# Kernel tuning notes

Measured on AMD Instinct MI355X. Metric: run time of the kernel, lower is better.

## Reference

```python
import jax, jax.numpy as jnp
import numpy as np

D_CONV = 4
DT_RANK = 64
D_STATE = 16

def silu(v):
    return v * jax.nn.sigmoid(v)

def setup_inputs() -> dict:
    key = jax.random.key(0)
    ks = jax.random.split(key, 10)
    B, L, d_model, d_inner = 2, 2048, 1024, 2048
    def nrm(k, shape, scale):
        return jax.random.normal(k, shape, dtype=jnp.float32) * scale
    A = jnp.tile(jnp.arange(1, D_STATE + 1, dtype=jnp.float32), (d_inner, 1))
    return {
        'x': nrm(ks[0], (B, L, d_model), 1.0),
        'W_in': nrm(ks[1], (d_model, 2 * d_inner), d_model ** -0.5),
        'conv_w': nrm(ks[2], (d_inner, D_CONV), D_CONV ** -0.5),
        'conv_b': nrm(ks[3], (d_inner,), 0.02),
        'W_x': nrm(ks[4], (d_inner, DT_RANK + 2 * D_STATE), d_inner ** -0.5),
        'W_dt': nrm(ks[5], (DT_RANK, d_inner), DT_RANK ** -0.5),
        'b_dt': nrm(ks[6], (d_inner,), 0.02),
        'A_log': jnp.log(A),
        'D': jnp.ones((d_inner,), dtype=jnp.float32),
        'W_out': nrm(ks[7], (d_inner, d_model), d_inner ** -0.5),
    }

def reference(x, W_in, conv_w, conv_b, W_x, W_dt, b_dt, A_log, D, W_out):
    B, L, _ = x.shape
    d_inner = W_dt.shape[1]
    # input projection and gate split
    xz = x @ W_in                                   # [B, L, 2*d_inner]
    xb, z = jnp.split(xz, 2, axis=-1)
    # causal depthwise conv1d (pad left d_conv-1, then first L outputs)
    xp = jnp.pad(xb, ((0, 0), (D_CONV - 1, 0), (0, 0)))
    xc = sum(xp[:, k:k + L, :] * conv_w[:, k] for k in range(D_CONV)) + conv_b
    xb = silu(xc)                                   # [B, L, d_inner]
    # data-dependent SSM parameters
    x_dbl = xb @ W_x                                # [B, L, dt_rank + 2*d_state]
    dt_low, Bm, Cm = jnp.split(x_dbl, [DT_RANK, DT_RANK + D_STATE], axis=-1)
    dt = jax.nn.softplus(dt_low @ W_dt + b_dt)      # [B, L, d_inner]
    A = -jnp.exp(A_log)                             # [d_inner, d_state]

    def step(h, inp):
        dt_t, B_t, C_t, x_t = inp                   # [B,d_inner],[B,n],[B,n],[B,d_inner]
        dA = jnp.exp(A * dt_t[..., None])           # [B, d_inner, d_state]
        h = h * dA + (x_t * dt_t)[..., None] * B_t[:, None, :]
        y = jnp.einsum('bdn,bn->bd', h, C_t)
        return h, y

    xs = (dt.swapaxes(0, 1), Bm.swapaxes(0, 1), Cm.swapaxes(0, 1), xb.swapaxes(0, 1))
    h0 = jnp.zeros((B, d_inner, D_STATE), dtype=x.dtype)
    _, ys = jax.lax.scan(step, h0, xs)              # ys: [L, B, d_inner]
    y = ys.swapaxes(0, 1) + xb * D
    out = y * silu(z)
    return out @ W_out
```

## Files before the change

kernel.cpp:

```cpp
#include <hip/hip_runtime.h>
#include <hip/hip_bf16.h>


#define BATCH   2
#define SEQLEN  2048
#define DMODEL  1024
#define DINNER  2048
#define DCONV   4
#define DTRANK  64
#define DSTATE  16
#define BL      (BATCH * SEQLEN)
#define NXZ     (2 * DINNER)
#define XDBL_N  (DTRANK + 2 * DSTATE)
#define LCH     32
#define NCHUNK  (SEQLEN / LCH)
#define KSPLIT  8
#define KC      (DINNER / KSPLIT)
#define KS_OUT  4
#define KCO     (DINNER / KS_OUT)
#define KS_XD   8
#define KCX     (DINNER / KS_XD)
#define XDP     128

typedef __bf16 bf16x8 __attribute__((ext_vector_type(8)));
typedef __bf16 bf16x4 __attribute__((ext_vector_type(4)));
typedef float  floatx4 __attribute__((ext_vector_type(4)));

__device__ __forceinline__ float silu_f(float v) {
    return v / (1.f + __expf(-v));
}

__device__ __forceinline__ float softplus_f(float v) {
    return (v > 20.f) ? v : __logf(1.f + __expf(v));
}

__device__ __forceinline__ float fast_exp2(float v) {
    return __builtin_amdgcn_exp2f(v);
}

__device__ __forceinline__ void gload_lds16(const __bf16* g, __bf16* l) {
    __builtin_amdgcn_global_load_lds(
        (const __attribute__((address_space(1))) void*)g,
        (__attribute__((address_space(3))) void*)l, 16, 0, 0);
}

#define VMW(n) asm volatile("s_waitcnt vmcnt(" #n ")" ::: "memory")
#define BARX() __builtin_amdgcn_s_barrier()

template <int BUF, int QA>
__device__ __forceinline__ void rdA(const char* rA, bf16x8 (&aF)[4][2]) {
#pragma unroll
    for (int j = 0; j < 4; ++j) {
        aF[j][0] = *(const bf16x8*)(rA + BUF * 65536 + ((QA * 4 + j) * 2 + 0) * 1024);
        aF[j][1] = *(const bf16x8*)(rA + BUF * 65536 + ((QA * 4 + j) * 2 + 1) * 1024);
    }
}

template <int BUF, int QB>
__device__ __forceinline__ void rdB(const char* rB, bf16x8 (&bF)[2][2]) {
#pragma unroll
    for (int f = 0; f < 2; ++f) {
        bF[f][0] = *(const bf16x8*)(rB + BUF * 65536 + QB * 8192 + f * 2048 + 0);
        bF[f][1] = *(const bf16x8*)(rB + BUF * 65536 + QB * 8192 + f * 2048 + 1024);
    }
}

template <int QA, int QB>
__device__ __forceinline__ void mf16(const bf16x8 (&aF)[4][2], const bf16x8 (&bF)[2][2],
                                     floatx4 (&acc)[8][4]) {
    __builtin_amdgcn_s_setprio(1);
#pragma unroll
    for (int ks = 0; ks < 2; ++ks)
#pragma unroll
        for (int j = 0; j < 4; ++j)
#pragma unroll
            for (int f = 0; f < 2; ++f)
                acc[QA * 4 + j][QB * 2 + f] = __builtin_amdgcn_mfma_f32_16x16x32_bf16(
                    aF[j][ks], bF[f][ks], acc[QA * 4 + j][QB * 2 + f], 0, 0, 0);
    __builtin_amdgcn_s_setprio(0);
}

template <int BUF, int QA>
__device__ __forceinline__ void stA2(const __bf16* gAs, char* sm, int lda, int w, int t) {
    gload_lds16(gAs + (size_t)(QA * 64) * lda + t * 64,
                (__bf16*)(sm + BUF * 65536 + QA * 8192 + w * 1024));
    gload_lds16(gAs + (size_t)(128 + QA * 64) * lda + t * 64,
                (__bf16*)(sm + BUF * 65536 + 16384 + QA * 8192 + w * 1024));
}

template <int BUF, int QB>
__device__ __forceinline__ void stB2(const __bf16* gBs, char* sm, int lda, int w, int t) {
    gload_lds16(gBs + (size_t)(QB * 32) * lda + t * 64,
                (__bf16*)(sm + BUF * 65536 + 32768 + QB * 8192 + w * 1024));
    gload_lds16(gBs + (size_t)(128 + QB * 32) * lda + t * 64,
                (__bf16*)(sm + BUF * 65536 + 32768 + 16384 + QB * 8192 + w * 1024));
}

template <int EPI>
__global__ __launch_bounds__(512, 2) void gemm_bt_256(
    const __bf16* __restrict__ A,
    const __bf16* __restrict__ BT,
    void* __restrict__ Cv,
    int M, int N, int K, int lda,
    const float* __restrict__ bias)
{
    __shared__ __align__(16) char smem[131072];

    const int tid  = threadIdx.x;
    const int w    = tid >> 6;
    const int lane = tid & 63;

    const int cpx = gridDim.x >> 3;
    const int swz = (blockIdx.x & 7) * cpx + (blockIdx.x >> 3);
    const int ntn = N >> 8;
    const int row0 = (swz / ntn) << 8;
    const int col0 = (swz % ntn) << 8;
    const int kbase = blockIdx.y * K;

    const int P     = tid;
    const int rr    = (P >> 2) & 15;
    const int qq    = (P & 3) ^ (2 * ((P >> 5) & 1));
    const int colE  = (((P >> 6) & 1) * 4 + qq) * 8;
    const int rgP   = P >> 7;
    const int rowAu = rgP * 16 + rr;
    const int rowBu = (rgP >> 1) * 64 + (rgP & 1) * 16 + rr;

    const __bf16* gAs = A  + (size_t)(row0 + rowAu) * lda + kbase + colE;
    const __bf16* gBs = BT + (size_t)(col0 + rowBu) * lda + kbase + colE;
    char* sm = smem;

    const int lsw = ((lane & 15) * 4 + ((lane >> 4) ^ (2 * ((lane >> 3) & 1)))) * 16;
    const char* rA = smem + (w >> 2) * 16384 + lsw;
    const char* rB = smem + 32768 + ((w & 3) >> 1) * 16384 + ((w & 3) & 1) * 4096 + lsw;

    floatx4 acc[8][4];
#pragma unroll
    for (int i = 0; i < 8; ++i)
#pragma unroll
        for (int j = 0; j < 4; ++j)
            acc[i][j] = (floatx4){0.f, 0.f, 0.f, 0.f};
    bf16x8 aF[4][2], bF[2][2];

    const int NT = K >> 6;
    const int NI = NT >> 1;

    stA2<0, 0>(gAs, sm, lda, w, 0);
    stB2<0, 0>(gBs, sm, lda, w, 0);
    stB2<0, 1>(gBs, sm, lda, w, 0);
    stA2<0, 1>(gAs, sm, lda, w, 0);
    stA2<1, 0>(gAs, sm, lda, w, 1);
    stB2<1, 1>(gBs, sm, lda, w, 1);
    VMW(6);
    BARX();

    for (int i = 0; i < NI - 1; ++i) {
        const int t1 = 2 * i + 1, t2 = 2 * i + 2, t3 = 2 * i + 3;
        rdA<0, 0>(rA, aF); rdB<0, 0>(rB, bF);
        stB2<1, 0>(gBs, sm, lda, w, t1);
        BARX(); mf16<0, 0>(aF, bF, acc); BARX();
        rdB<0, 1>(rB, bF);
        stA2<1, 1>(gAs, sm, lda, w, t1);
        BARX(); mf16<0, 1>(aF, bF, acc); VMW(8); BARX();
        rdA<0, 1>(rA, aF);
        stA2<0, 0>(gAs, sm, lda, w, t2);
        BARX(); mf16<1, 1>(aF, bF, acc); BARX();
        rdB<0, 0>(rB, bF);
        stB2<0, 1>(gBs, sm, lda, w, t2);
        BARX(); mf16<1, 0>(aF, bF, acc); VMW(6); BARX();
        rdA<1, 0>(rA, aF); rdB<1, 0>(rB, bF);
        stB2<0, 0>(gBs, sm, lda, w, t2);
        BARX(); mf16<0, 0>(aF, bF, acc); BARX();
        rdB<1, 1>(rB, bF);
        stA2<0, 1>(gAs, sm, lda, w, t2);
        BARX(); mf16<0, 1>(aF, bF, acc); VMW(8); BARX();
        rdA<1, 1>(rA, aF);
        stA2<1, 0>(gAs, sm, lda, w, t3);
        BARX(); mf16<1, 1>(aF, bF, acc); BARX();
        rdB<1, 0>(rB, bF);
        stB2<1, 1>(gBs, sm, lda, w, t3);
        BARX(); mf16<1, 0>(aF, bF, acc); VMW(6); BARX();
    }
    {
        const int t1 = NT - 1;
        rdA<0, 0>(rA, aF); rdB<0, 0>(rB, bF);
        stB2<1, 0>(gBs, sm, lda, w, t1);
        BARX(); mf16<0, 0>(aF, bF, acc); BARX();
        rdB<0, 1>(rB, bF);
        stA2<1, 1>(gAs, sm, lda, w, t1);
        BARX(); mf16<0, 1>(aF, bF, acc); VMW(8); BARX();
        rdA<0, 1>(rA, aF);
        BARX(); mf16<1, 1>(aF, bF, acc); BARX();
        rdB<0, 0>(rB, bF);
        BARX(); mf16<1, 0>(aF, bF, acc); VMW(2); BARX();
        rdA<1, 0>(rA, aF); rdB<1, 0>(rB, bF);
        BARX(); mf16<0, 0>(aF, bF, acc); BARX();
        rdB<1, 1>(rB, bF);
        BARX(); mf16<0, 1>(aF, bF, acc); VMW(0); BARX();
        rdA<1, 1>(rA, aF);
        BARX(); mf16<1, 1>(aF, bF, acc); BARX();
        rdB<1, 0>(rB, bF);
        BARX(); mf16<1, 0>(aF, bF, acc);
    }

    const int lrow = lane & 15, quad = lane >> 4;

    if (EPI == 2 || EPI == 3) {
        __syncthreads();
#pragma unroll
        for (int fi = 0; fi < 8; ++fi) {
#pragma unroll
            for (int cf = 0; cf < 4; ++cf) {
                const int lc = (w & 3) * 64 + cf * 16 + lrow;
                const float bv = (EPI == 3) ? bias[col0 + lc] : 0.f;
#pragma unroll
                for (int r = 0; r < 4; ++r) {
                    const int lr = (w >> 2) * 128 + fi * 16 + quad * 4 + r;
                    float v = acc[fi][cf][r];
                    if (EPI == 3) v = softplus_f(v + bv);
                    const int ck = (lc >> 3) ^ ((lr >> 2) & 7);
                    *(__bf16*)(smem + lr * 512 + ck * 16 + (lc & 7) * 2) = (__bf16)v;
                }
            }
        }
        __syncthreads();
#pragma unroll
        for (int it = 0; it < 16; ++it) {
            const int row = it * 16 + w * 2 + (lane >> 5);
            const int cr  = lane & 31;
            const int ck  = cr ^ ((row >> 2) & 7);
            bf16x8 v = *(const bf16x8*)(smem + row * 512 + ck * 16);
            *(bf16x8*)((__bf16*)Cv + (size_t)(row0 + row) * N + col0 + cr * 8) = v;
        }
    } else {
        const size_t cofs = (size_t)blockIdx.y * (size_t)M * (size_t)N;
        const int rbase = row0 + (w >> 2) * 128;
        const int cbase = col0 + (w & 3) * 64;
#pragma unroll
        for (int fi = 0; fi < 8; ++fi) {
#pragma unroll
            for (int cf = 0; cf < 4; ++cf) {
                const int col = cbase + cf * 16 + lrow;
                const float bv = (EPI == 1) ? bias[col] : 0.f;
#pragma unroll
                for (int r = 0; r < 4; ++r) {
                    const int row = rbase + fi * 16 + quad * 4 + r;
                    float v = acc[fi][cf][r];
                    if (EPI == 1) v = softplus_f(v + bv);
                    ((float*)Cv)[cofs + (size_t)row * N + col] = v;
                }
            }
        }
    }
    (void)M;
}

__global__ __launch_bounds__(256) void out_reduce(
    const float* __restrict__ parts, float* __restrict__ out)
{
    const size_t i = ((size_t)blockIdx.x * 256 + threadIdx.x) * 4;
    floatx4 s = *(const floatx4*)(parts + i);
#pragma unroll
    for (int kz = 1; kz < KS_OUT; ++kz)
        s += *(const floatx4*)(parts + (size_t)kz * BL * DMODEL + i);
    *(floatx4*)(out + i) = s;
}

template <int EPI>
__global__ __launch_bounds__(256) void gemm_r64(
    const __bf16* __restrict__ A,
    const __bf16* __restrict__ BT,
    void* __restrict__ Cv,
    int M, int N, int K,
    const float* __restrict__ bias)
{
    __shared__ __bf16 Asm[64 * 32];
    __shared__ __bf16 Bsm[128 * 32];

    const int tid  = threadIdx.x;
    const int w    = tid >> 6;
    const int lane = tid & 63;
    const int lrow = lane & 15;
    const int quad = lane >> 4;
    const int row0 = blockIdx.y * 64;
    const int col0 = blockIdx.x * 128;
    const int wc   = w * 32;

    const int ldr = tid >> 2;
    const int ldk = (tid & 3) * 8;
    const __bf16* gA = A  + (size_t)(row0 + ldr) * K + ldk;
    const __bf16* gB = BT + (size_t)(col0 + ldr) * K + ldk;
    const size_t half = (size_t)64 * K;
    __bf16* lA0 = Asm + w * 512;
    __bf16* lB0 = Bsm + w * 512;
    __bf16* lB1 = Bsm + 2048 + w * 512;

    floatx4 acc[4][2];
#pragma unroll
    for (int i = 0; i < 4; ++i)
#pragma unroll
        for (int j = 0; j < 2; ++j)
            acc[i][j] = (floatx4){0.f, 0.f, 0.f, 0.f};

    for (int k0 = 0; k0 < K; k0 += 32) {
        gload_lds16(gA, lA0);
        gload_lds16(gB, lB0);
        gload_lds16(gB + half, lB1);
        gA += 32; gB += 32;
        __syncthreads();

        bf16x8 af[4], bf[2];
#pragma unroll
        for (int t = 0; t < 4; ++t)
            af[t] = *(const bf16x8*)(Asm + (t * 16 + lrow) * 32 + quad * 8);
#pragma unroll
        for (int u = 0; u < 2; ++u)
            bf[u] = *(const bf16x8*)(Bsm + (wc + u * 16 + lrow) * 32 + quad * 8);

#pragma unroll
        for (int ti = 0; ti < 4; ++ti)
#pragma unroll
            for (int tj = 0; tj < 2; ++tj)
                acc[ti][tj] = __builtin_amdgcn_mfma_f32_16x16x32_bf16(
                    af[ti], bf[tj], acc[ti][tj], 0, 0, 0);
        __syncthreads();
    }

#pragma unroll
    for (int ti = 0; ti < 4; ++ti) {
#pragma unroll
        for (int tj = 0; tj < 2; ++tj) {
            int col = col0 + wc + tj * 16 + lrow;
            float bv = (EPI == 1 || EPI == 3) ? bias[col] : 0.f;
#pragma unroll
            for (int r = 0; r < 4; ++r) {
                int row = row0 + ti * 16 + quad * 4 + r;
                float v = acc[ti][tj][r];
                if (EPI == 1 || EPI == 3) v = softplus_f(v + bv);
                if (EPI == 2 || EPI == 3)
                    ((__bf16*)Cv)[(size_t)row * N + col] = (__bf16)v;
                else
                    ((float*)Cv)[(size_t)row * N + col] = v;
            }
        }
    }
}

__global__ __launch_bounds__(256) void xdbl_gemm(
    const __bf16* __restrict__ A,
    const __bf16* __restrict__ BT,
    float* __restrict__ parts)
{
    __shared__ __bf16 Asm[64 * 32];
    __shared__ __bf16 Bsm[128 * 32];

    const int tid  = threadIdx.x;
    const int w    = tid >> 6;
    const int lane = tid & 63;
    const int lrow = lane & 15;
    const int quad = lane >> 4;
    const int row0 = blockIdx.x * 64;
    const int kbeg = blockIdx.y * KCX;
    const int wc   = w * 32;

    const int ldr = tid >> 2;
    const int ldk = (tid & 3) * 8;
    const __bf16* gA = A  + (size_t)(row0 + ldr) * DINNER + kbeg + ldk;
    const __bf16* gB = BT + (size_t)ldr * DINNER + kbeg + ldk;
    const size_t half = (size_t)64 * DINNER;
    __bf16* lA0 = Asm + w * 512;
    __bf16* lB0 = Bsm + w * 512;
    __bf16* lB1 = Bsm + 2048 + w * 512;

    floatx4 acc[4][2];
#pragma unroll
    for (int i = 0; i < 4; ++i)
#pragma unroll
        for (int j = 0; j < 2; ++j)
            acc[i][j] = (floatx4){0.f, 0.f, 0.f, 0.f};

    for (int k0 = 0; k0 < KCX; k0 += 32) {
        gload_lds16(gA, lA0);
        gload_lds16(gB, lB0);
        gload_lds16(gB + half, lB1);
        gA += 32; gB += 32;
        __syncthreads();

        bf16x8 af[4], bf[2];
#pragma unroll
        for (int t = 0; t < 4; ++t)
            af[t] = *(const bf16x8*)(Asm + (t * 16 + lrow) * 32 + quad * 8);
#pragma unroll
        for (int u = 0; u < 2; ++u)
            bf[u] = *(const bf16x8*)(Bsm + (wc + u * 16 + lrow) * 32 + quad * 8);

#pragma unroll
        for (int ti = 0; ti < 4; ++ti)
#pragma unroll
            for (int tj = 0; tj < 2; ++tj)
                acc[ti][tj] = __builtin_amdgcn_mfma_f32_16x16x32_bf16(
                    af[ti], bf[tj], acc[ti][tj], 0, 0, 0);
        __syncthreads();
    }

    const size_t base = (size_t)blockIdx.y * BL * XDP;
#pragma unroll
    for (int ti = 0; ti < 4; ++ti) {
#pragma unroll
        for (int tj = 0; tj < 2; ++tj) {
            int col = wc + tj * 16 + lrow;
#pragma unroll
            for (int r = 0; r < 4; ++r) {
                int row = row0 + ti * 16 + quad * 4 + r;
                parts[base + (size_t)row * XDP + col] = acc[ti][tj][r];
            }
        }
    }
}

__global__ __launch_bounds__(256) void xdbl_reduce2(
    const float* __restrict__ parts, float* __restrict__ xdbl,
    __bf16* __restrict__ dtlow16)
{
    const int i4  = blockIdx.x * 256 + threadIdx.x;
    const int row = i4 / 24;
    const int c4  = i4 - row * 24;
    const float* p = parts + (size_t)row * XDP + c4 * 4;
    floatx4 s = *(const floatx4*)p;
#pragma unroll
    for (int kz = 1; kz < KS_XD; ++kz)
        s += *(const floatx4*)(p + (size_t)kz * BL * XDP);
    *(floatx4*)(xdbl + (size_t)row * XDBL_N + c4 * 4) = s;
    if (c4 < 16) {
        bf16x4 o = {(__bf16)s.x, (__bf16)s.y, (__bf16)s.z, (__bf16)s.w};
        *(bf16x4*)(dtlow16 + (size_t)row * DTRANK + c4 * 4) = o;
    }
}

#define NB_CAST  ((BL * DMODEL / 4) / 256)
#define NB_WIN   ((NXZ / 32) * (DMODEL / 32))
#define NB_WOUT  ((DMODEL / 32) * (DINNER / 32))
#define NB_WDT   ((DINNER / 32) * (DTRANK / 32))
#define NB_CW    ((DCONV * DINNER) / 256)

__device__ __forceinline__ void transpose_tile(
    const float* __restrict__ src, __bf16* __restrict__ dst, int R, int Cc,
    int bx, int by, int tid, float* tile)
{
    int tx = tid & 31, ty = tid >> 5;
    int c0 = bx * 32, r0 = by * 32;
#pragma unroll
    for (int i = 0; i < 32; i += 8)
        tile[(ty + i) * 33 + tx] = src[(size_t)(r0 + ty + i) * Cc + c0 + tx];
    __syncthreads();
#pragma unroll
    for (int i = 0; i < 32; i += 8)
        dst[(size_t)(c0 + ty + i) * R + r0 + tx] = (__bf16)tile[tx * 33 + ty + i];
}

__global__ __launch_bounds__(256) void prep_kernel(
    const float* __restrict__ x,
    const float* __restrict__ W_in,
    const float* __restrict__ W_out,
    const float* __restrict__ W_dt,
    const float* __restrict__ conv_w,
    __bf16* __restrict__ xb16,
    __bf16* __restrict__ WiT16,
    __bf16* __restrict__ WoT16,
    __bf16* __restrict__ WdtT16,
    float* __restrict__ cwT)
{
    __shared__ float tile[32 * 33];
    const int tid = threadIdx.x;
    int bid = blockIdx.x;

    if (bid < NB_CAST) {
        long i = ((long)bid * 256 + tid) * 4;
        float4 v = *(const float4*)(x + i);
        bf16x4 o = {(__bf16)v.x, (__bf16)v.y, (__bf16)v.z, (__bf16)v.w};
        *(bf16x4*)(xb16 + i) = o;
        return;
    }
    bid -= NB_CAST;
    if (bid < NB_WIN) {
        transpose_tile(W_in, WiT16, DMODEL, NXZ,
                       bid % (NXZ / 32), bid / (NXZ / 32), tid, tile);
        return;
    }
    bid -= NB_WIN;
    if (bid < NB_WOUT) {
        transpose_tile(W_out, WoT16, DINNER, DMODEL,
                       bid % (DMODEL / 32), bid / (DMODEL / 32), tid, tile);
        return;
    }
    bid -= NB_WOUT;
    if (bid < NB_WDT) {
        transpose_tile(W_dt, WdtT16, DTRANK, DINNER,
                       bid % (DINNER / 32), bid / (DINNER / 32), tid, tile);
        return;
    }
    bid -= NB_WDT;
    {
        int i = bid * 256 + tid;
        int k = i / DINNER, d = i % DINNER;
        cwT[i] = conv_w[d * DCONV + k];
    }
}

#define NB_CONV  ((BL / 64) * KSPLIT)
#define NB_WXT   ((DINNER / 32) * (XDBL_N / 32))

__global__ __launch_bounds__(256) void conv_prep(
    const __bf16* __restrict__ xz16,
    const float* __restrict__ cwT,
    const float* __restrict__ cb,
    const float* __restrict__ W_x,
    __bf16* __restrict__ xc16,
    __bf16* __restrict__ WxT16)
{
    __shared__ float tile[32 * 33];
    const int tid = threadIdx.x;
    const int bid = blockIdx.x;

    if (bid >= NB_CONV) {
        const int b2 = bid - NB_CONV;
        transpose_tile(W_x, WxT16, DINNER, XDBL_N,
                       b2 % (XDBL_N / 32), b2 / (XDBL_N / 32), tid, tile);
        return;
    }

    const int row0 = (bid >> 3) * 64;
    const int kbeg = (bid & 7) * KC;
    const int ct = (tid & 31) * 8;
    const int rt = (tid >> 5) * 8;
    const int d  = kbeg + ct;

    float wreg[DCONV][8];
#pragma unroll
    for (int k = 0; k < DCONV; ++k) {
        float4 a = *(const float4*)(cwT + k * DINNER + d);
        float4 b = *(const float4*)(cwT + k * DINNER + d + 4);
        wreg[k][0]=a.x; wreg[k][1]=a.y; wreg[k][2]=a.z; wreg[k][3]=a.w;
        wreg[k][4]=b.x; wreg[k][5]=b.y; wreg[k][6]=b.z; wreg[k][7]=b.w;
    }
    float bias8[8];
    {
        float4 a = *(const float4*)(cb + d);
        float4 b = *(const float4*)(cb + d + 4);
        bias8[0]=a.x; bias8[1]=a.y; bias8[2]=a.z; bias8[3]=a.w;
        bias8[4]=b.x; bias8[5]=b.y; bias8[6]=b.z; bias8[7]=b.w;
    }

    const bf16x8 zero = {};
    bf16x8 win[DCONV];
    const int tloc0 = (int)((row0 + rt) & (SEQLEN - 1));
#pragma unroll
    for (int j = 0; j < DCONV - 1; ++j)
        win[j] = (tloc0 - 3 + j >= 0)
            ? *(const bf16x8*)(xz16 + (size_t)(row0 + rt - 3 + j) * NXZ + d)
            : zero;

    for (int i = 0; i < 8; ++i) {
        size_t r = (size_t)row0 + rt + i;
        win[DCONV - 1] = *(const bf16x8*)(xz16 + r * NXZ + d);
        bf16x8 o;
#pragma unroll
        for (int j = 0; j < 8; ++j) {
            float acc = bias8[j];
#pragma unroll
            for (int k = 0; k < DCONV; ++k)
                acc += (float)win[k][j] * wreg[k][j];
            o[j] = (__bf16)silu_f(acc);
        }
        *(bf16x8*)(xc16 + r * DINNER + d) = o;
#pragma unroll
        for (int k = 0; k < DCONV - 1; ++k)
            win[k] = win[k + 1];
    }
}

__global__ __launch_bounds__(256) void scan_pass1(
    const __bf16* __restrict__ dt16,
    const __bf16* __restrict__ xc16,
    const float* __restrict__ xdbl,
    const float* __restrict__ A_log,
    float* __restrict__ sums_h,
    float* __restrict__ sums_p)
{
    __shared__ __align__(16) float Bs[LCH][16];

    const int d  = blockIdx.x * 256 + threadIdx.x;
    const int bc = blockIdx.y;
    const int b  = bc / NCHUNK, c = bc % NCHUNK;
    const long r0 = (long)b * SEQLEN + (long)c * LCH;

    if (threadIdx.x < LCH * 4) {
        const int row = threadIdx.x >> 2, c4 = threadIdx.x & 3;
        *(float4*)&Bs[row][c4 * 4] =
            *(const float4*)(xdbl + (size_t)(r0 + row) * XDBL_N + DTRANK + c4 * 4);
    }

    float Ad[DSTATE];
    {
        const float4* al = (const float4*)(A_log + d * DSTATE);
#pragma unroll
        for (int q = 0; q < 4; ++q) {
            float4 v = al[q];
            Ad[q * 4 + 0] = -__expf(v.x) * 1.44269504f;
            Ad[q * 4 + 1] = -__expf(v.y) * 1.44269504f;
            Ad[q * 4 + 2] = -__expf(v.z) * 1.44269504f;
            Ad[q * 4 + 3] = -__expf(v.w) * 1.44269504f;
        }
    }
    __syncthreads();

    float h[DSTATE] = {};
    float Sdt = 0.f;

#pragma unroll 4
    for (int t = 0; t < LCH; ++t) {
        long r = r0 + t;
        float dtv = (float)dt16[r * DINNER + d];
        float xv  = (float)xc16[r * DINNER + d];
        float xdt = xv * dtv;
        Sdt += dtv;
        const float4* bv = (const float4*)Bs[t];
        float4 B0 = bv[0], B1 = bv[1], B2 = bv[2], B3 = bv[3];
        const float Bn[DSTATE] = {B0.x,B0.y,B0.z,B0.w, B1.x,B1.y,B1.z,B1.w,
                                  B2.x,B2.y,B2.z,B2.w, B3.x,B3.y,B3.z,B3.w};
#pragma unroll
        for (int n = 0; n < DSTATE; ++n) {
            float dA = fast_exp2(Ad[n] * dtv);
            h[n] = h[n] * dA + xdt * Bn[n];
        }
    }

    const long rowbase = (long)bc * DSTATE;
#pragma unroll
    for (int n = 0; n < DSTATE; ++n) {
        sums_h[(rowbase + n) * DINNER + d] = h[n];
        sums_p[(rowbase + n) * DINNER + d] = fast_exp2(Ad[n] * Sdt);
    }
}

__global__ __launch_bounds__(256) void scan_combine(
    float* __restrict__ sums_h, float* __restrict__ sums_p)
{
    int u = blockIdx.x * 256 + threadIdx.x;
    int d = u & (DINNER - 1);
    int n = (u >> 11) & (DSTATE - 1);
    int b = u >> 15;
    float hg = 0.f;
    for (int c = 0; c < NCHUNK; ++c) {
        long row = (long)(b * NCHUNK + c) * DSTATE + n;
        float p  = sums_p[row * DINNER + d];
        float hl = sums_h[row * DINNER + d];
        sums_p[row * DINNER + d] = hg;
        hg = p * hg + hl;
    }
}

__global__ __launch_bounds__(256) void scan_pass3(
    const __bf16* __restrict__ dt16,
    const __bf16* __restrict__ xc16,
    const float* __restrict__ xdbl,
    const float* __restrict__ A_log,
    const __bf16* __restrict__ xz16,
    const float* __restrict__ sums_p,
    const float* __restrict__ Dp,
    __bf16* __restrict__ gated)
{
    __shared__ __align__(16) float BCs[LCH][32];

    const int d  = blockIdx.x * 256 + threadIdx.x;
    const int bc = blockIdx.y;
    const int b  = bc / NCHUNK, c = bc % NCHUNK;
    const long r0 = (long)b * SEQLEN + (long)c * LCH;

    {
        const int row = threadIdx.x >> 3, c4 = threadIdx.x & 7;
        *(float4*)&BCs[row][c4 * 4] =
            *(const float4*)(xdbl + (size_t)(r0 + row) * XDBL_N + DTRANK + c4 * 4);
    }

    float Ad[DSTATE];
    {
        const float4* al = (const float4*)(A_log + d * DSTATE);
#pragma unroll
        for (int q = 0; q < 4; ++q) {
            float4 v = al[q];
            Ad[q * 4 + 0] = -__expf(v.x) * 1.44269504f;
            Ad[q * 4 + 1] = -__expf(v.y) * 1.44269504f;
            Ad[q * 4 + 2] = -__expf(v.z) * 1.44269504f;
            Ad[q * 4 + 3] = -__expf(v.w) * 1.44269504f;
        }
    }

    float h[DSTATE];
    const long rowbase = (long)bc * DSTATE;
#pragma unroll
    for (int n = 0; n < DSTATE; ++n)
        h[n] = sums_p[(rowbase + n) * DINNER + d];

    const float Dv = Dp[d];
    __syncthreads();

#pragma unroll 4
    for (int t = 0; t < LCH; ++t) {
        long r = r0 + t;
        float dtv = (float)dt16[r * DINNER + d];
        float xv  = (float)xc16[r * DINNER + d];
        float xdt = xv * dtv;
        const float4* bv = (const float4*)BCs[t];
        float4 B0 = bv[0], B1 = bv[1], B2 = bv[2], B3 = bv[3];
        float4 C0 = bv[4], C1 = bv[5], C2 = bv[6], C3 = bv[7];
        const float Bn[DSTATE] = {B0.x,B0.y,B0.z,B0.w, B1.x,B1.y,B1.z,B1.w,
                                  B2.x,B2.y,B2.z,B2.w, B3.x,B3.y,B3.z,B3.w};
        const float Cn[DSTATE] = {C0.x,C0.y,C0.z,C0.w, C1.x,C1.y,C1.z,C1.w,
                                  C2.x,C2.y,C2.z,C2.w, C3.x,C3.y,C3.z,C3.w};
        float y = 0.f;
#pragma unroll
        for (int n = 0; n < DSTATE; ++n) {
            float dA = fast_exp2(Ad[n] * dtv);
            h[n] = h[n] * dA + xdt * Bn[n];
            y += h[n] * Cn[n];
        }
        float z = (float)xz16[r * NXZ + DINNER + d];
        float yy = y + xv * Dv;
        gated[r * DINNER + d] = (__bf16)(yy * silu_f(z));
    }
}

extern "C" void kernel_launch(void* const* d_in, const int* in_sizes, int n_in,
                              void* d_out, int out_size, void* d_ws, size_t ws_size,
                              hipStream_t stream) {
    const float* x      = (const float*)d_in[0];
    const float* W_in   = (const float*)d_in[1];
    const float* conv_w = (const float*)d_in[2];
    const float* conv_b = (const float*)d_in[3];
    const float* W_x    = (const float*)d_in[4];
    const float* W_dt   = (const float*)d_in[5];
    const float* b_dt   = (const float*)d_in[6];
    const float* A_log  = (const float*)d_in[7];
    const float* Dp     = (const float*)d_in[8];
    const float* W_out  = (const float*)d_in[9];
    float* out = (float*)d_out;

    __bf16* xz16    = (__bf16*)d_ws;
    __bf16* xc16    = xz16 + (long)BL * NXZ;
    __bf16* dt16    = xc16 + (long)BL * DINNER;
    __bf16* gated16 = dt16 + (long)BL * DINNER;
    __bf16* WoT16   = gated16 + (long)BL * DINNER;
    __bf16* WdtT16  = WoT16 + (long)DINNER * DMODEL;
    __bf16* dtlow16 = WdtT16 + (long)DINNER * DTRANK;
    __bf16* xb16    = dtlow16 + (long)BL * DTRANK;
    __bf16* WiT16   = xb16 + (long)BL * DMODEL;
    float*  xdbl    = (float*)(WiT16 + (long)NXZ * DMODEL);
    float*  cwT     = xdbl + (long)BL * XDBL_N;
    float*  scratch = cwT + (long)DCONV * DINNER;
    float*  sums_h  = scratch;
    float*  sums_p  = scratch + (long)BATCH * NCHUNK * DSTATE * DINNER;
    __bf16* WxT16 = xb16;
    float* outparts = (float*)d_ws;

    dim3 blk(256);

    prep_kernel<<<dim3(NB_CAST + NB_WIN + NB_WOUT + NB_WDT + NB_CW), blk, 0, stream>>>(
        x, W_in, W_out, W_dt, conv_w, xb16, WiT16, WoT16, WdtT16, cwT);

    gemm_bt_256<2><<<dim3((BL / 256) * (NXZ / 256)), dim3(512), 0, stream>>>(
        xb16, WiT16, xz16, BL, NXZ, DMODEL, DMODEL, nullptr);

    conv_prep<<<dim3(NB_CONV + NB_WXT), blk, 0, stream>>>(
        xz16, cwT, conv_b, W_x, xc16, WxT16);

    xdbl_gemm<<<dim3(BL / 64, KS_XD), blk, 0, stream>>>(xc16, WxT16, scratch);
    xdbl_reduce2<<<dim3((BL * 24) / 256), blk, 0, stream>>>(scratch, xdbl, dtlow16);

    gemm_r64<3><<<dim3(DINNER / 128, BL / 64), blk, 0, stream>>>(
        dtlow16, WdtT16, dt16, BL, DINNER, DTRANK, b_dt);

    {
        dim3 grid1(DINNER / 256, BATCH * NCHUNK);
        scan_pass1<<<grid1, blk, 0, stream>>>(dt16, xc16, xdbl, A_log, sums_h, sums_p);
        scan_combine<<<dim3((BATCH * DSTATE * DINNER) / 256), blk, 0, stream>>>(
            sums_h, sums_p);
        scan_pass3<<<grid1, blk, 0, stream>>>(dt16, xc16, xdbl, A_log, xz16,
                                              sums_p, Dp, gated16);
    }
    gemm_bt_256<0><<<dim3((BL / 256) * (DMODEL / 256), KS_OUT), dim3(512), 0, stream>>>(
        gated16, WoT16, outparts, BL, DMODEL, KCO, DINNER, nullptr);
    out_reduce<<<dim3((BL * DMODEL) / 1024), blk, 0, stream>>>(outparts, out);

    (void)in_sizes; (void)n_in; (void)out_size; (void)ws_size;
}
```

Before: 276.8 us.

## Fuse causal conv into x_dbl GEMM and move W_x transpose to prep

The depthwise causal conv + SiLU is computed inside the x_dbl split-K GEMM blocks, and the result is staged in LDS as the A operand while still being written to global memory for the scan. This removes the separate conv kernel launch and the global re-read of the conv output for the GEMM. The W_x transpose moves into the prep kernel, and its buffer moves to the scan scratch area. The larger LDS footprint may reduce occupancy.

```diff
diff --git a/kernel.cpp b/kernel.cpp
--- a/kernel.cpp
+++ b/kernel.cpp
@@ -18,9 +18,8 @@
 #define KC      (DINNER / KSPLIT)
 #define KS_OUT  4
 #define KCO     (DINNER / KS_OUT)
-#define KS_XD   8
-#define KCX     (DINNER / KS_XD)
 #define XDP     128
+#define ALDS    264
 
 typedef __bf16 bf16x8 __attribute__((ext_vector_type(8)));
 typedef __bf16 bf16x4 __attribute__((ext_vector_type(4)));
@@ -345,12 +344,15 @@
     }
 }
 
-__global__ __launch_bounds__(256) void xdbl_gemm(
-    const __bf16* __restrict__ A,
-    const __bf16* __restrict__ BT,
+__global__ __launch_bounds__(256) void xdbl_fused2(
+    const __bf16* __restrict__ xz16,
+    const float* __restrict__ cwT,
+    const float* __restrict__ cb,
+    const __bf16* __restrict__ WxT,
+    __bf16* __restrict__ xc16,
     float* __restrict__ parts)
 {
-    __shared__ __bf16 Asm[64 * 32];
+    __shared__ __bf16 Acv[64 * ALDS];
     __shared__ __bf16 Bsm[128 * 32];
 
     const int tid  = threadIdx.x;
@@ -359,15 +361,65 @@
     const int lrow = lane & 15;
     const int quad = lane >> 4;
     const int row0 = blockIdx.x * 64;
-    const int kbeg = blockIdx.y * KCX;
+    const int kz   = blockIdx.y;
+    const int kbeg = kz * KC;
     const int wc   = w * 32;
+
+    {
+        const int ct = (tid & 31) * 8;
+        const int rt = (tid >> 5) * 8;
+        const int d  = kbeg + ct;
+
+        float wreg[DCONV][8];
+#pragma unroll
+        for (int k = 0; k < DCONV; ++k) {
+            float4 a = *(const float4*)(cwT + k * DINNER + d);
+            float4 b = *(const float4*)(cwT + k * DINNER + d + 4);
+            wreg[k][0]=a.x; wreg[k][1]=a.y; wreg[k][2]=a.z; wreg[k][3]=a.w;
+            wreg[k][4]=b.x; wreg[k][5]=b.y; wreg[k][6]=b.z; wreg[k][7]=b.w;
+        }
+        float bias8[8];
+        {
+            float4 a = *(const float4*)(cb + d);
+            float4 b = *(const float4*)(cb + d + 4);
+            bias8[0]=a.x; bias8[1]=a.y; bias8[2]=a.z; bias8[3]=a.w;
+            bias8[4]=b.x; bias8[5]=b.y; bias8[6]=b.z; bias8[7]=b.w;
+        }
+
+        const bf16x8 zero = {};
+        bf16x8 win[DCONV];
+        const int tloc0 = (int)((row0 + rt) & (SEQLEN - 1));
+#pragma unroll
+        for (int j = 0; j < DCONV - 1; ++j)
+            win[j] = (tloc0 - 3 + j >= 0)
+                ? *(const bf16x8*)(xz16 + (size_t)(row0 + rt - 3 + j) * NXZ + d)
+                : zero;
+
+        for (int i = 0; i < 8; ++i) {
+            size_t r = (size_t)row0 + rt + i;
+            win[DCONV - 1] = *(const bf16x8*)(xz16 + r * NXZ + d);
+            bf16x8 o;
+#pragma unroll
+            for (int j = 0; j < 8; ++j) {
+                float acc = bias8[j];
+#pragma unroll
+                for (int k = 0; k < DCONV; ++k)
+                    acc += (float)win[k][j] * wreg[k][j];
+                o[j] = (__bf16)silu_f(acc);
+            }
+            *(bf16x8*)(xc16 + r * DINNER + d) = o;
+            *(bf16x8*)(Acv + (rt + i) * ALDS + ct) = o;
+#pragma unroll
+            for (int k = 0; k < DCONV - 1; ++k)
+                win[k] = win[k + 1];
+        }
+    }
+    __syncthreads();
 
     const int ldr = tid >> 2;
     const int ldk = (tid & 3) * 8;
-    const __bf16* gA = A  + (size_t)(row0 + ldr) * DINNER + kbeg + ldk;
-    const __bf16* gB = BT + (size_t)ldr * DINNER + kbeg + ldk;
+    const __bf16* gB = WxT + (size_t)ldr * DINNER + kbeg + ldk;
     const size_t half = (size_t)64 * DINNER;
-    __bf16* lA0 = Asm + w * 512;
     __bf16* lB0 = Bsm + w * 512;
     __bf16* lB1 = Bsm + 2048 + w * 512;
 
@@ -378,17 +430,16 @@
         for (int j = 0; j < 2; ++j)
             acc[i][j] = (floatx4){0.f, 0.f, 0.f, 0.f};
 
-    for (int k0 = 0; k0 < KCX; k0 += 32) {
-        gload_lds16(gA, lA0);
+    for (int k0 = 0; k0 < KC; k0 += 32) {
         gload_lds16(gB, lB0);
         gload_lds16(gB + half, lB1);
-        gA += 32; gB += 32;
+        gB += 32;
         __syncthreads();
 
         bf16x8 af[4], bf[2];
 #pragma unroll
         for (int t = 0; t < 4; ++t)
-            af[t] = *(const bf16x8*)(Asm + (t * 16 + lrow) * 32 + quad * 8);
+            af[t] = *(const bf16x8*)(Acv + (t * 16 + lrow) * ALDS + k0 + quad * 8);
 #pragma unroll
         for (int u = 0; u < 2; ++u)
             bf[u] = *(const bf16x8*)(Bsm + (wc + u * 16 + lrow) * 32 + quad * 8);
@@ -402,7 +453,7 @@
         __syncthreads();
     }
 
-    const size_t base = (size_t)blockIdx.y * BL * XDP;
+    const size_t base = (size_t)kz * BL * XDP;
 #pragma unroll
     for (int ti = 0; ti < 4; ++ti) {
 #pragma unroll
@@ -427,7 +478,7 @@
     const float* p = parts + (size_t)row * XDP + c4 * 4;
     floatx4 s = *(const floatx4*)p;
 #pragma unroll
-    for (int kz = 1; kz < KS_XD; ++kz)
+    for (int kz = 1; kz < KSPLIT; ++kz)
         s += *(const floatx4*)(p + (size_t)kz * BL * XDP);
     *(floatx4*)(xdbl + (size_t)row * XDBL_N + c4 * 4) = s;
     if (c4 < 16) {
@@ -441,6 +492,7 @@
 #define NB_WOUT  ((DMODEL / 32) * (DINNER / 32))
 #define NB_WDT   ((DINNER / 32) * (DTRANK / 32))
 #define NB_CW    ((DCONV * DINNER) / 256)
+#define NB_WXT   ((DINNER / 32) * (XDBL_N / 32))
 
 __device__ __forceinline__ void transpose_tile(
     const float* __restrict__ src, __bf16* __restrict__ dst, int R, int Cc,
@@ -462,11 +514,13 @@
     const float* __restrict__ W_in,
     const float* __restrict__ W_out,
     const float* __restrict__ W_dt,
+    const float* __restrict__ W_x,
     const float* __restrict__ conv_w,
     __bf16* __restrict__ xb16,
     __bf16* __restrict__ WiT16,
     __bf16* __restrict__ WoT16,
     __bf16* __restrict__ WdtT16,
+    __bf16* __restrict__ WxT16,
     float* __restrict__ cwT)
 {
     __shared__ float tile[32 * 33];
@@ -499,82 +553,16 @@
         return;
     }
     bid -= NB_WDT;
-    {
+    if (bid < NB_CW) {
         int i = bid * 256 + tid;
         int k = i / DINNER, d = i % DINNER;
         cwT[i] = conv_w[d * DCONV + k];
-    }
-}
-
-#define NB_CONV  ((BL / 64) * KSPLIT)
-#define NB_WXT   ((DINNER / 32) * (XDBL_N / 32))
-
-__global__ __launch_bounds__(256) void conv_prep(
-    const __bf16* __restrict__ xz16,
-    const float* __restrict__ cwT,
-    const float* __restrict__ cb,
-    const float* __restrict__ W_x,
-    __bf16* __restrict__ xc16,
-    __bf16* __restrict__ WxT16)
-{
-    __shared__ float tile[32 * 33];
-    const int tid = threadIdx.x;
-    const int bid = blockIdx.x;
-
-    if (bid >= NB_CONV) {
-        const int b2 = bid - NB_CONV;
+        return;
+    }
+    bid -= NB_CW;
+    {
         transpose_tile(W_x, WxT16, DINNER, XDBL_N,
-                       b2 % (XDBL_N / 32), b2 / (XDBL_N / 32), tid, tile);
-        return;
-    }
-
-    const int row0 = (bid >> 3) * 64;
-    const int kbeg = (bid & 7) * KC;
-    const int ct = (tid & 31) * 8;
-    const int rt = (tid >> 5) * 8;
-    const int d  = kbeg + ct;
-
-    float wreg[DCONV][8];
-#pragma unroll
-    for (int k = 0; k < DCONV; ++k) {
-        float4 a = *(const float4*)(cwT + k * DINNER + d);
-        float4 b = *(const float4*)(cwT + k * DINNER + d + 4);
-        wreg[k][0]=a.x; wreg[k][1]=a.y; wreg[k][2]=a.z; wreg[k][3]=a.w;
-        wreg[k][4]=b.x; wreg[k][5]=b.y; wreg[k][6]=b.z; wreg[k][7]=b.w;
-    }
-    float bias8[8];
-    {
-        float4 a = *(const float4*)(cb + d);
-        float4 b = *(const float4*)(cb + d + 4);
-        bias8[0]=a.x; bias8[1]=a.y; bias8[2]=a.z; bias8[3]=a.w;
-        bias8[4]=b.x; bias8[5]=b.y; bias8[6]=b.z; bias8[7]=b.w;
-    }
-
-    const bf16x8 zero = {};
-    bf16x8 win[DCONV];
-    const int tloc0 = (int)((row0 + rt) & (SEQLEN - 1));
-#pragma unroll
-    for (int j = 0; j < DCONV - 1; ++j)
-        win[j] = (tloc0 - 3 + j >= 0)
-            ? *(const bf16x8*)(xz16 + (size_t)(row0 + rt - 3 + j) * NXZ + d)
-            : zero;
-
-    for (int i = 0; i < 8; ++i) {
-        size_t r = (size_t)row0 + rt + i;
-        win[DCONV - 1] = *(const bf16x8*)(xz16 + r * NXZ + d);
-        bf16x8 o;
-#pragma unroll
-        for (int j = 0; j < 8; ++j) {
-            float acc = bias8[j];
-#pragma unroll
-            for (int k = 0; k < DCONV; ++k)
-                acc += (float)win[k][j] * wreg[k][j];
-            o[j] = (__bf16)silu_f(acc);
-        }
-        *(bf16x8*)(xc16 + r * DINNER + d) = o;
-#pragma unroll
-        for (int k = 0; k < DCONV - 1; ++k)
-            win[k] = win[k + 1];
+                       bid % (XDBL_N / 32), bid / (XDBL_N / 32), tid, tile);
     }
 }
 
@@ -759,21 +747,20 @@
     float*  scratch = cwT + (long)DCONV * DINNER;
     float*  sums_h  = scratch;
     float*  sums_p  = scratch + (long)BATCH * NCHUNK * DSTATE * DINNER;
-    __bf16* WxT16 = xb16;
+    __bf16* WxT16 = (__bf16*)sums_p;
     float* outparts = (float*)d_ws;
 
     dim3 blk(256);
 
-    prep_kernel<<<dim3(NB_CAST + NB_WIN + NB_WOUT + NB_WDT + NB_CW), blk, 0, stream>>>(
-        x, W_in, W_out, W_dt, conv_w, xb16, WiT16, WoT16, WdtT16, cwT);
+    prep_kernel<<<dim3(NB_CAST + NB_WIN + NB_WOUT + NB_WDT + NB_CW + NB_WXT),
+                  blk, 0, stream>>>(
+        x, W_in, W_out, W_dt, W_x, conv_w, xb16, WiT16, WoT16, WdtT16, WxT16, cwT);
 
     gemm_bt_256<2><<<dim3((BL / 256) * (NXZ / 256)), dim3(512), 0, stream>>>(
         xb16, WiT16, xz16, BL, NXZ, DMODEL, DMODEL, nullptr);
 
-    conv_prep<<<dim3(NB_CONV + NB_WXT), blk, 0, stream>>>(
-        xz16, cwT, conv_b, W_x, xc16, WxT16);
-
-    xdbl_gemm<<<dim3(BL / 64, KS_XD), blk, 0, stream>>>(xc16, WxT16, scratch);
+    xdbl_fused2<<<dim3(BL / 64, KSPLIT), blk, 0, stream>>>(
+        xz16, cwT, conv_b, WxT16, xc16, scratch);
     xdbl_reduce2<<<dim3((BL * 24) / 256), blk, 0, stream>>>(scratch, xdbl, dtlow16);
 
     gemm_r64<3><<<dim3(DINNER / 128, BL / 64), blk, 0, stream>>>(
```

New measurement: 277.5 us. No clear change (+0.2%).
